# Kernel optimization log

Hardware: AMD Instinct MI355X
Metric: run time of the kernel (lower is better)

Reference implementation:

```python
import jax, jax.numpy as jnp
import numpy as np

B, N, M, C, H = 4, 8192, 8192, 512, 8
D = C // H  # head_dim = 64

def setup_inputs() -> dict:
    key = jax.random.key(0)
    ks = jax.random.split(key, 10)
    s = 1.0 / np.sqrt(C)
    return {
        "x": jax.random.normal(ks[0], (B, N, C), dtype=jnp.float32),
        "y": jax.random.normal(ks[1], (B, M, C), dtype=jnp.float32),
        "Wq": jax.random.normal(ks[2], (C, C), dtype=jnp.float32) * s,
        "bq": jax.random.normal(ks[3], (C,), dtype=jnp.float32) * s,
        "Wk": jax.random.normal(ks[4], (C, C), dtype=jnp.float32) * s,
        "bk": jax.random.normal(ks[5], (C,), dtype=jnp.float32) * s,
        "Wv": jax.random.normal(ks[6], (C, C), dtype=jnp.float32) * s,
        "bv": jax.random.normal(ks[7], (C,), dtype=jnp.float32) * s,
        "Wp": jax.random.normal(ks[8], (C, C), dtype=jnp.float32) * s,
        "bp": jax.random.normal(ks[9], (C,), dtype=jnp.float32) * s,
    }

def reference(x, y, Wq, bq, Wk, bk, Wv, bv, Wp, bp):
    # project and split heads: (B, S, C) -> (B, H, S, D)
    def heads(t, W, b, S):
        return (t @ W + b).reshape(B, S, H, D).transpose(0, 2, 1, 3)
    q = jax.nn.softmax(heads(x, Wq, bq, N), axis=-1)   # (B,H,N,D)
    k = jax.nn.softmax(heads(y, Wk, bk, M), axis=-1)   # (B,H,M,D)
    v = heads(y, Wv, bv, M)                             # (B,H,M,D)
    # denom: (q * sum_m k).sum_d, clamped
    ksum = jnp.sum(k, axis=2, keepdims=True)            # (B,H,1,D)
    denom = jnp.maximum(jnp.sum(q * ksum, axis=-1, keepdims=True), 1e-6)  # (B,H,N,1)
    # reassociated k^T @ v: (B,H,D,D), then q @ (k^T v)
    kv = jnp.einsum("bhmd,bhme->bhde", k, v)
    out = jnp.einsum("bhnd,bhde->bhne", q, kv) / denom + q  # (B,H,N,D)
    out = out.transpose(0, 2, 1, 3).reshape(B, N, C)
    return out @ Wp + bp  # dropout rate 0.0 -> identity
```

## Files before the change

### kernel.cpp

```cpp
#include <hip/hip_runtime.h>

typedef __bf16 bf16_t;
typedef __bf16 bf16x4 __attribute__((ext_vector_type(4)));
typedef __bf16 bf16x8 __attribute__((ext_vector_type(8)));
typedef float f32x4 __attribute__((ext_vector_type(4)));

#define AS1 __attribute__((address_space(1)))
#define AS3 __attribute__((address_space(3)))

__device__ __forceinline__ void gll16(const void* g, void* l) {
  __builtin_amdgcn_global_load_lds((AS1 void*)g, (AS3 void*)l, 16, 0, 0);
}

template <int ACT, bool TRANS>
__launch_bounds__(256, 2)
__global__ void gemm_k(const bf16_t* __restrict__ A, const bf16_t* __restrict__ BT,
                       const float* __restrict__ bias, void* __restrict__ Cout) {
  __shared__ __align__(16) bf16_t As[128 * 64];
  __shared__ __align__(16) bf16_t Bs[128 * 64];
  const int tid = threadIdx.x;
  const int lane = tid & 63, wid = tid >> 6;
  const int wr = wid >> 1, wc = wid & 1;
  const int rowbase = blockIdx.x * 128, colbase = blockIdx.y * 128;

  f32x4 zero = {0.f, 0.f, 0.f, 0.f};
  f32x4 acc[4][4];
#pragma unroll
  for (int i = 0; i < 4; ++i)
#pragma unroll
    for (int j = 0; j < 4; ++j) acc[i][j] = zero;

  const int srow = wid * 8 + (lane >> 3);
  const int scol = (lane & 7) * 8;
  const size_t abase = (size_t)(rowbase + srow) * 512 + scol;
  const size_t bbase = (size_t)(colbase + srow) * 512 + scol;
  bf16_t* lA = As + wid * 512;
  bf16_t* lB = Bs + wid * 512;

  for (int k0 = 0; k0 < 512; k0 += 64) {
#pragma unroll
    for (int i = 0; i < 4; ++i) {
      gll16(A + abase + (size_t)i * (32 * 512) + k0, lA + i * 2048);
      gll16(BT + bbase + (size_t)i * (32 * 512) + k0, lB + i * 2048);
    }
    __syncthreads();
#pragma unroll
    for (int kk = 0; kk < 64; kk += 32) {
      bf16x8 af[4], bfr[4];
#pragma unroll
      for (int ri = 0; ri < 4; ++ri)
        af[ri] = *(const bf16x8*)&As[(wr * 64 + ri * 16 + (lane & 15)) * 64 + kk + (lane >> 4) * 8];
#pragma unroll
      for (int ci = 0; ci < 4; ++ci)
        bfr[ci] = *(const bf16x8*)&Bs[(wc * 64 + ci * 16 + (lane & 15)) * 64 + kk + (lane >> 4) * 8];
#pragma unroll
      for (int ri = 0; ri < 4; ++ri)
#pragma unroll
        for (int ci = 0; ci < 4; ++ci)
          acc[ri][ci] = __builtin_amdgcn_mfma_f32_16x16x32_bf16(af[ri], bfr[ci], acc[ri][ci], 0, 0, 0);
    }
    __syncthreads();
  }

  float bb[4];
#pragma unroll
  for (int ci = 0; ci < 4; ++ci) bb[ci] = bias[colbase + wc * 64 + ci * 16 + (lane & 15)];
#pragma unroll
  for (int ri = 0; ri < 4; ++ri)
#pragma unroll
    for (int ci = 0; ci < 4; ++ci)
#pragma unroll
      for (int r = 0; r < 4; ++r) acc[ri][ci][r] += bb[ci];

  if (ACT == 1) {
#pragma unroll
    for (int ri = 0; ri < 4; ++ri) {
#pragma unroll
      for (int r = 0; r < 4; ++r) {
        float m = fmaxf(fmaxf(acc[ri][0][r], acc[ri][1][r]), fmaxf(acc[ri][2][r], acc[ri][3][r]));
        m = fmaxf(m, __shfl_xor(m, 1));
        m = fmaxf(m, __shfl_xor(m, 2));
        m = fmaxf(m, __shfl_xor(m, 4));
        m = fmaxf(m, __shfl_xor(m, 8));
        float s = 0.f;
#pragma unroll
        for (int ci = 0; ci < 4; ++ci) {
          float p = __expf(acc[ri][ci][r] - m);
          acc[ri][ci][r] = p;
          s += p;
        }
        s += __shfl_xor(s, 1);
        s += __shfl_xor(s, 2);
        s += __shfl_xor(s, 4);
        s += __shfl_xor(s, 8);
        float rcp = 1.0f / s;
#pragma unroll
        for (int ci = 0; ci < 4; ++ci) acc[ri][ci][r] *= rcp;
      }
    }
  }

  const int lr = (lane >> 4) * 4, lc = lane & 15;
#pragma unroll
  for (int ri = 0; ri < 4; ++ri)
#pragma unroll
    for (int ci = 0; ci < 4; ++ci)
#pragma unroll
      for (int r = 0; r < 4; ++r) {
        int gm = rowbase + wr * 64 + ri * 16 + lr + r;
        int c = colbase + wc * 64 + ci * 16 + lc;
        if (TRANS) {
          size_t idx = ((size_t)((gm >> 13) * 8 + (c >> 6)) * 64 + (c & 63)) * 8192 + (gm & 8191);
          ((bf16_t*)Cout)[idx] = (bf16_t)acc[ri][ci][r];
        } else {
          size_t idx = (size_t)gm * 512 + c;
          if (ACT == 2)
            ((float*)Cout)[idx] = acc[ri][ci][r];
          else
            ((bf16_t*)Cout)[idx] = (bf16_t)acc[ri][ci][r];
        }
      }
}

__launch_bounds__(256, 2)
__global__ void kv2_k(const bf16_t* __restrict__ Kt, const bf16_t* __restrict__ Vt,
                      float* __restrict__ kv, float* __restrict__ ksum) {
  __shared__ __align__(16) bf16_t Ks[64 * 64];
  __shared__ __align__(16) bf16_t Vs[64 * 64];
  const int bh = blockIdx.x >> 4, sp = blockIdx.x & 15;
  const int tid = threadIdx.x, lane = tid & 63, wid = tid >> 6;
  const size_t base = (size_t)bh * 64 * 8192;
  const int m0 = sp * 512;
  const int srow = wid * 8 + (lane >> 3);
  const int scol = (lane & 7) * 8;

  f32x4 zero = {0.f, 0.f, 0.f, 0.f};
  f32x4 acc[4], accs[4];
#pragma unroll
  for (int i = 0; i < 4; ++i) { acc[i] = zero; accs[i] = zero; }
  bf16x8 ones;
#pragma unroll
  for (int j = 0; j < 8; ++j) ones[j] = (bf16_t)1.0f;

  for (int c = 0; c < 8; ++c) {
    const int mc = m0 + c * 64;
#pragma unroll
    for (int i = 0; i < 2; ++i) {
      size_t g = base + (size_t)(srow + i * 32) * 8192 + mc + scol;
      gll16(Kt + g, Ks + wid * 512 + i * 2048);
      gll16(Vt + g, Vs + wid * 512 + i * 2048);
    }
    __syncthreads();
#pragma unroll
    for (int kk = 0; kk < 64; kk += 32) {
      bf16x8 af[4];
#pragma unroll
      for (int ri = 0; ri < 4; ++ri)
        af[ri] = *(const bf16x8*)&Ks[(ri * 16 + (lane & 15)) * 64 + kk + (lane >> 4) * 8];
      bf16x8 bfr = *(const bf16x8*)&Vs[(wid * 16 + (lane & 15)) * 64 + kk + (lane >> 4) * 8];
#pragma unroll
      for (int ri = 0; ri < 4; ++ri)
        acc[ri] = __builtin_amdgcn_mfma_f32_16x16x32_bf16(af[ri], bfr, acc[ri], 0, 0, 0);
      if (wid == 0) {
#pragma unroll
        for (int ri = 0; ri < 4; ++ri)
          accs[ri] = __builtin_amdgcn_mfma_f32_16x16x32_bf16(af[ri], ones, accs[ri], 0, 0, 0);
      }
    }
    __syncthreads();
  }

  const int lr = (lane >> 4) * 4, lc = lane & 15;
#pragma unroll
  for (int ri = 0; ri < 4; ++ri)
#pragma unroll
    for (int r = 0; r < 4; ++r)
      atomicAdd(&kv[((size_t)bh * 64 + ri * 16 + lr + r) * 64 + wid * 16 + lc], acc[ri][r]);
  if (wid == 0 && lc == 0) {
#pragma unroll
    for (int ri = 0; ri < 4; ++ri)
#pragma unroll
      for (int r = 0; r < 4; ++r)
        atomicAdd(&ksum[bh * 64 + ri * 16 + lr + r], accs[ri][r]);
  }
}

__global__ void build_kvB(const float* __restrict__ kv, const float* __restrict__ ksum,
                          bf16_t* __restrict__ kvB) {
  int i = blockIdx.x * 256 + threadIdx.x;
  if (i >= 32 * 80 * 64) return;
  int k = i & 63;
  int col = (i >> 6) % 80;
  int bh = i / (80 * 64);
  float v = 0.f;
  if (col < 64)
    v = kv[(size_t)(bh * 64 + k) * 64 + col];
  else if (col == 64)
    v = ksum[bh * 64 + k];
  kvB[i] = (bf16_t)v;
}

__launch_bounds__(256, 2)
__global__ void attn_k(const bf16_t* __restrict__ Q, const bf16_t* __restrict__ kvB,
                       bf16_t* __restrict__ attn) {
  __shared__ __align__(16) bf16_t As[128 * 64];
  const int rt = blockIdx.x;
  const int h = blockIdx.y;
  const int b = rt >> 6;
  const int bh = b * 8 + h;
  const int tid = threadIdx.x, lane = tid & 63, wid = tid >> 6;
  const int srow = wid * 8 + (lane >> 3);
  const int scol = (lane & 7) * 8;
#pragma unroll
  for (int i = 0; i < 4; ++i)
    gll16(Q + (size_t)(rt * 128 + srow + i * 32) * 512 + h * 64 + scol, As + wid * 512 + i * 2048);

  f32x4 zero = {0.f, 0.f, 0.f, 0.f};
  f32x4 acc[2][5];
#pragma unroll
  for (int i = 0; i < 2; ++i)
#pragma unroll
    for (int j = 0; j < 5; ++j) acc[i][j] = zero;
  __syncthreads();

  const bf16_t* Bb = kvB + (size_t)bh * (80 * 64);
#pragma unroll
  for (int kk = 0; kk < 64; kk += 32) {
    bf16x8 af[2];
#pragma unroll
    for (int ri = 0; ri < 2; ++ri)
      af[ri] = *(const bf16x8*)&As[(wid * 32 + ri * 16 + (lane & 15)) * 64 + kk + (lane >> 4) * 8];
#pragma unroll
    for (int ci = 0; ci < 5; ++ci) {
      bf16x8 bfr = *(const bf16x8*)&Bb[(ci * 16 + (lane & 15)) * 64 + kk + (lane >> 4) * 8];
#pragma unroll
      for (int ri = 0; ri < 2; ++ri)
        acc[ri][ci] = __builtin_amdgcn_mfma_f32_16x16x32_bf16(af[ri], bfr, acc[ri][ci], 0, 0, 0);
    }
  }

  const int lr = (lane >> 4) * 4, lc = lane & 15;
#pragma unroll
  for (int ri = 0; ri < 2; ++ri)
#pragma unroll
    for (int r = 0; r < 4; ++r) {
      float dn = __shfl(acc[ri][4][r], lane & 48);
      dn = fmaxf(dn, 1e-6f);
      float rinv = 1.0f / dn;
      int rl = wid * 32 + ri * 16 + lr + r;
#pragma unroll
      for (int ci = 0; ci < 4; ++ci) {
        int e = ci * 16 + lc;
        float qv = (float)As[rl * 64 + e];
        float o = acc[ri][ci][r] * rinv + qv;
        attn[(size_t)(rt * 128 + rl) * 512 + h * 64 + e] = (bf16_t)o;
      }
    }
}

__global__ void cvt_k(const float* __restrict__ in, bf16_t* __restrict__ out, int n4) {
  int i = blockIdx.x * blockDim.x + threadIdx.x;
  if (i < n4) {
    float4 v = ((const float4*)in)[i];
    bf16x4 o;
    o[0] = (bf16_t)v.x;
    o[1] = (bf16_t)v.y;
    o[2] = (bf16_t)v.z;
    o[3] = (bf16_t)v.w;
    ((bf16x4*)out)[i] = o;
  }
}

__global__ void wtrans_k(const float* __restrict__ W, bf16_t* __restrict__ WT) {
  int i = blockIdx.x * 256 + threadIdx.x;
  int n = i >> 9, k = i & 511;
  WT[i] = (bf16_t)W[k * 512 + n];
}

__global__ void zero_k(float* __restrict__ p, int n) {
  int i = blockIdx.x * 256 + threadIdx.x;
  if (i < n) p[i] = 0.f;
}

extern "C" void kernel_launch(void* const* d_in, const int* in_sizes, int n_in,
                              void* d_out, int out_size, void* d_ws, size_t ws_size,
                              hipStream_t stream) {
  (void)in_sizes; (void)n_in; (void)out_size; (void)ws_size;
  const float* x  = (const float*)d_in[0];
  const float* y  = (const float*)d_in[1];
  const float* Wq = (const float*)d_in[2];
  const float* bq = (const float*)d_in[3];
  const float* Wk = (const float*)d_in[4];
  const float* bk = (const float*)d_in[5];
  const float* Wv = (const float*)d_in[6];
  const float* bv = (const float*)d_in[7];
  const float* Wp = (const float*)d_in[8];
  const float* bp = (const float*)d_in[9];
  float* out = (float*)d_out;

  char* ws = (char*)d_ws;
  const size_t MB = 1024 * 1024;
  bf16_t* xbf = (bf16_t*)(ws + 0);
  bf16_t* ybf = (bf16_t*)(ws + 32 * MB);
  bf16_t* Qb  = (bf16_t*)(ws + 64 * MB);
  bf16_t* Kt  = (bf16_t*)(ws + 96 * MB);
  bf16_t* Vt  = (bf16_t*)(ws + 128 * MB);
  bf16_t* WqT = (bf16_t*)(ws + 160 * MB);
  bf16_t* WkT = WqT + 512 * 512;
  bf16_t* WvT = WkT + 512 * 512;
  bf16_t* WpT = WvT + 512 * 512;
  float* kv   = (float*)(ws + 163 * MB);
  float* ksum = kv + 32 * 64 * 64;
  bf16_t* kvB = (bf16_t*)(ws + 164 * MB);
  bf16_t* attn = xbf;

  cvt_k<<<16384, 256, 0, stream>>>(x, xbf, 4194304);
  cvt_k<<<16384, 256, 0, stream>>>(y, ybf, 4194304);
  wtrans_k<<<1024, 256, 0, stream>>>(Wq, WqT);
  wtrans_k<<<1024, 256, 0, stream>>>(Wk, WkT);
  wtrans_k<<<1024, 256, 0, stream>>>(Wv, WvT);
  wtrans_k<<<1024, 256, 0, stream>>>(Wp, WpT);

  dim3 gg(256, 4);
  gemm_k<1, false><<<gg, 256, 0, stream>>>(xbf, WqT, bq, Qb);
  gemm_k<1, true><<<gg, 256, 0, stream>>>(ybf, WkT, bk, Kt);
  gemm_k<0, true><<<gg, 256, 0, stream>>>(ybf, WvT, bv, Vt);

  zero_k<<<(133120 + 255) / 256, 256, 0, stream>>>(kv, 133120);
  kv2_k<<<512, 256, 0, stream>>>(Kt, Vt, kv, ksum);
  build_kvB<<<(32 * 80 * 64) / 256, 256, 0, stream>>>(kv, ksum, kvB);

  attn_k<<<dim3(256, 8), 256, 0, stream>>>(Qb, kvB, attn);

  gemm_k<2, false><<<gg, 256, 0, stream>>>(attn, WpT, bp, out);
}
```

Measured before the change: 357.3 us.

## Merge prep and QKV launches, replace kv atomics with split partials, vectorize K/V stores

The six conversion and transpose kernels become one prep kernel, and the three QKV projection GEMMs become one launch with a z-dimension selecting Q, K or V. The kv reduction now writes per-split partial buffers that build_kvB sums, which removes the atomics and the zero-init kernel. The transposed K/V epilogue now stores four consecutive bf16 values as one bf16x4 write instead of scalar scattered stores. This cuts launch overhead and store inefficiency, at the cost of a larger partial-sum workspace and a 16-way read in build_kvB.

```diff
diff --git a/kernel.cpp b/kernel.cpp
--- a/kernel.cpp
+++ b/kernel.cpp
@@ -13,15 +13,16 @@
 }
 
 template <int ACT, bool TRANS>
-__launch_bounds__(256, 2)
-__global__ void gemm_k(const bf16_t* __restrict__ A, const bf16_t* __restrict__ BT,
-                       const float* __restrict__ bias, void* __restrict__ Cout) {
+__device__ __forceinline__ void gemm_core(const bf16_t* __restrict__ A,
+                                          const bf16_t* __restrict__ BT,
+                                          const float* __restrict__ bias,
+                                          void* __restrict__ Cout,
+                                          int rowbase, int colbase) {
   __shared__ __align__(16) bf16_t As[128 * 64];
   __shared__ __align__(16) bf16_t Bs[128 * 64];
   const int tid = threadIdx.x;
   const int lane = tid & 63, wid = tid >> 6;
   const int wr = wid >> 1, wc = wid & 1;
-  const int rowbase = blockIdx.x * 128, colbase = blockIdx.y * 128;
 
   f32x4 zero = {0.f, 0.f, 0.f, 0.f};
   f32x4 acc[4][4];
@@ -101,30 +102,63 @@
   }
 
   const int lr = (lane >> 4) * 4, lc = lane & 15;
-#pragma unroll
-  for (int ri = 0; ri < 4; ++ri)
-#pragma unroll
-    for (int ci = 0; ci < 4; ++ci)
-#pragma unroll
-      for (int r = 0; r < 4; ++r) {
-        int gm = rowbase + wr * 64 + ri * 16 + lr + r;
+  if (TRANS) {
+#pragma unroll
+    for (int ri = 0; ri < 4; ++ri)
+#pragma unroll
+      for (int ci = 0; ci < 4; ++ci) {
+        bf16x4 pk;
+#pragma unroll
+        for (int r = 0; r < 4; ++r) pk[r] = (bf16_t)acc[ri][ci][r];
+        int gm0 = rowbase + wr * 64 + ri * 16 + lr;
         int c = colbase + wc * 64 + ci * 16 + lc;
-        if (TRANS) {
-          size_t idx = ((size_t)((gm >> 13) * 8 + (c >> 6)) * 64 + (c & 63)) * 8192 + (gm & 8191);
-          ((bf16_t*)Cout)[idx] = (bf16_t)acc[ri][ci][r];
-        } else {
+        size_t idx = ((size_t)((gm0 >> 13) * 8 + (c >> 6)) * 64 + (c & 63)) * 8192 + (gm0 & 8191);
+        *(bf16x4*)&((bf16_t*)Cout)[idx] = pk;
+      }
+  } else {
+#pragma unroll
+    for (int ri = 0; ri < 4; ++ri)
+#pragma unroll
+      for (int ci = 0; ci < 4; ++ci)
+#pragma unroll
+        for (int r = 0; r < 4; ++r) {
+          int gm = rowbase + wr * 64 + ri * 16 + lr + r;
+          int c = colbase + wc * 64 + ci * 16 + lc;
           size_t idx = (size_t)gm * 512 + c;
           if (ACT == 2)
             ((float*)Cout)[idx] = acc[ri][ci][r];
           else
             ((bf16_t*)Cout)[idx] = (bf16_t)acc[ri][ci][r];
         }
-      }
+  }
+}
+
+__launch_bounds__(256, 2)
+__global__ void qkv_k(const bf16_t* __restrict__ xbf, const bf16_t* __restrict__ ybf,
+                      const bf16_t* __restrict__ WqT, const bf16_t* __restrict__ WkT,
+                      const bf16_t* __restrict__ WvT,
+                      const float* __restrict__ bq, const float* __restrict__ bk,
+                      const float* __restrict__ bv,
+                      bf16_t* __restrict__ Qb, bf16_t* __restrict__ Kt,
+                      bf16_t* __restrict__ Vt) {
+  const int rowbase = blockIdx.x * 128, colbase = blockIdx.y * 128;
+  if (blockIdx.z == 0)
+    gemm_core<1, false>(xbf, WqT, bq, Qb, rowbase, colbase);
+  else if (blockIdx.z == 1)
+    gemm_core<1, true>(ybf, WkT, bk, Kt, rowbase, colbase);
+  else
+    gemm_core<0, true>(ybf, WvT, bv, Vt, rowbase, colbase);
+}
+
+__launch_bounds__(256, 2)
+__global__ void pgemm_k(const bf16_t* __restrict__ A, const bf16_t* __restrict__ BT,
+                        const float* __restrict__ bias, float* __restrict__ Cout) {
+  gemm_core<2, false>(A, BT, bias, Cout, blockIdx.x * 128, blockIdx.y * 128);
 }
 
 __launch_bounds__(256, 2)
 __global__ void kv2_k(const bf16_t* __restrict__ Kt, const bf16_t* __restrict__ Vt,
-                      float* __restrict__ kv, float* __restrict__ ksum) {
+                      float* __restrict__ kvp, float* __restrict__ ksp) {
   __shared__ __align__(16) bf16_t Ks[64 * 64];
   __shared__ __align__(16) bf16_t Vs[64 * 64];
   const int bh = blockIdx.x >> 4, sp = blockIdx.x & 15;
@@ -171,21 +205,22 @@
   }
 
   const int lr = (lane >> 4) * 4, lc = lane & 15;
+  float* o = kvp + ((size_t)sp * 32 + bh) * 4096;
 #pragma unroll
   for (int ri = 0; ri < 4; ++ri)
 #pragma unroll
     for (int r = 0; r < 4; ++r)
-      atomicAdd(&kv[((size_t)bh * 64 + ri * 16 + lr + r) * 64 + wid * 16 + lc], acc[ri][r]);
+      o[(ri * 16 + lr + r) * 64 + wid * 16 + lc] = acc[ri][r];
   if (wid == 0 && lc == 0) {
+    float* os = ksp + ((size_t)sp * 32 + bh) * 64;
 #pragma unroll
     for (int ri = 0; ri < 4; ++ri)
 #pragma unroll
-      for (int r = 0; r < 4; ++r)
-        atomicAdd(&ksum[bh * 64 + ri * 16 + lr + r], accs[ri][r]);
-  }
-}
-
-__global__ void build_kvB(const float* __restrict__ kv, const float* __restrict__ ksum,
+      for (int r = 0; r < 4; ++r) os[ri * 16 + lr + r] = accs[ri][r];
+  }
+}
+
+__global__ void build_kvB(const float* __restrict__ kvp, const float* __restrict__ ksp,
                           bf16_t* __restrict__ kvB) {
   int i = blockIdx.x * 256 + threadIdx.x;
   if (i >= 32 * 80 * 64) return;
@@ -193,10 +228,15 @@
   int col = (i >> 6) % 80;
   int bh = i / (80 * 64);
   float v = 0.f;
-  if (col < 64)
-    v = kv[(size_t)(bh * 64 + k) * 64 + col];
-  else if (col == 64)
-    v = ksum[bh * 64 + k];
+  if (col < 64) {
+#pragma unroll
+    for (int sp = 0; sp < 16; ++sp)
+      v += kvp[((size_t)sp * 32 + bh) * 4096 + k * 64 + col];
+  } else if (col == 64) {
+#pragma unroll
+    for (int sp = 0; sp < 16; ++sp)
+      v += ksp[((size_t)sp * 32 + bh) * 64 + k];
+  }
   kvB[i] = (bf16_t)v;
 }
 
@@ -258,28 +298,32 @@
     }
 }
 
-__global__ void cvt_k(const float* __restrict__ in, bf16_t* __restrict__ out, int n4) {
-  int i = blockIdx.x * blockDim.x + threadIdx.x;
-  if (i < n4) {
-    float4 v = ((const float4*)in)[i];
+__global__ void prep_k(const float* __restrict__ x, const float* __restrict__ y,
+                       const float* __restrict__ Wq, const float* __restrict__ Wk,
+                       const float* __restrict__ Wv, const float* __restrict__ Wp,
+                       bf16_t* __restrict__ xbf, bf16_t* __restrict__ ybf,
+                       bf16_t* __restrict__ WqT, bf16_t* __restrict__ WkT,
+                       bf16_t* __restrict__ WvT, bf16_t* __restrict__ WpT) {
+  int i = blockIdx.x * 256 + threadIdx.x;
+  if (i < 8388608) {
+    const float* src = (i < 4194304) ? x : y;
+    bf16_t* dst = (i < 4194304) ? xbf : ybf;
+    int j = (i < 4194304) ? i : i - 4194304;
+    float4 v = ((const float4*)src)[j];
     bf16x4 o;
     o[0] = (bf16_t)v.x;
     o[1] = (bf16_t)v.y;
     o[2] = (bf16_t)v.z;
     o[3] = (bf16_t)v.w;
-    ((bf16x4*)out)[i] = o;
-  }
-}
-
-__global__ void wtrans_k(const float* __restrict__ W, bf16_t* __restrict__ WT) {
-  int i = blockIdx.x * 256 + threadIdx.x;
-  int n = i >> 9, k = i & 511;
-  WT[i] = (bf16_t)W[k * 512 + n];
-}
-
-__global__ void zero_k(float* __restrict__ p, int n) {
-  int i = blockIdx.x * 256 + threadIdx.x;
-  if (i < n) p[i] = 0.f;
+    ((bf16x4*)dst)[j] = o;
+  } else {
+    int i2 = i - 8388608;
+    int w = i2 >> 18, j = i2 & 262143;
+    int n = j >> 9, k = j & 511;
+    const float* W = (w == 0) ? Wq : (w == 1) ? Wk : (w == 2) ? Wv : Wp;
+    bf16_t* WT = (w == 0) ? WqT : (w == 1) ? WkT : (w == 2) ? WvT : WpT;
+    WT[j] = (bf16_t)W[k * 512 + n];
+  }
 }
 
 extern "C" void kernel_launch(void* const* d_in, const int* in_sizes, int n_in,
@@ -309,28 +353,19 @@
   bf16_t* WkT = WqT + 512 * 512;
   bf16_t* WvT = WkT + 512 * 512;
   bf16_t* WpT = WvT + 512 * 512;
-  float* kv   = (float*)(ws + 163 * MB);
-  float* ksum = kv + 32 * 64 * 64;
-  bf16_t* kvB = (bf16_t*)(ws + 164 * MB);
+  float* kvp  = (float*)(ws + 163 * MB);
+  float* ksp  = (float*)(ws + 171 * MB);
+  bf16_t* kvB = (bf16_t*)(ws + 172 * MB);
   bf16_t* attn = xbf;
 
-  cvt_k<<<16384, 256, 0, stream>>>(x, xbf, 4194304);
-  cvt_k<<<16384, 256, 0, stream>>>(y, ybf, 4194304);
-  wtrans_k<<<1024, 256, 0, stream>>>(Wq, WqT);
-  wtrans_k<<<1024, 256, 0, stream>>>(Wk, WkT);
-  wtrans_k<<<1024, 256, 0, stream>>>(Wv, WvT);
-  wtrans_k<<<1024, 256, 0, stream>>>(Wp, WpT);
-
-  dim3 gg(256, 4);
-  gemm_k<1, false><<<gg, 256, 0, stream>>>(xbf, WqT, bq, Qb);
-  gemm_k<1, true><<<gg, 256, 0, stream>>>(ybf, WkT, bk, Kt);
-  gemm_k<0, true><<<gg, 256, 0, stream>>>(ybf, WvT, bv, Vt);
-
-  zero_k<<<(133120 + 255) / 256, 256, 0, stream>>>(kv, 133120);
-  kv2_k<<<512, 256, 0, stream>>>(Kt, Vt, kv, ksum);
-  build_kvB<<<(32 * 80 * 64) / 256, 256, 0, stream>>>(kv, ksum, kvB);
+  prep_k<<<36864, 256, 0, stream>>>(x, y, Wq, Wk, Wv, Wp, xbf, ybf, WqT, WkT, WvT, WpT);
+
+  qkv_k<<<dim3(256, 4, 3), 256, 0, stream>>>(xbf, ybf, WqT, WkT, WvT, bq, bk, bv, Qb, Kt, Vt);
+
+  kv2_k<<<512, 256, 0, stream>>>(Kt, Vt, kvp, ksp);
+  build_kvB<<<(32 * 80 * 64) / 256, 256, 0, stream>>>(kvp, ksp, kvB);
 
   attn_k<<<dim3(256, 8), 256, 0, stream>>>(Qb, kvB, attn);
 
-  gemm_k<2, false><<<gg, 256, 0, stream>>>(attn, WpT, bp, out);
-}
+  pgemm_k<<<dim3(256, 4), 256, 0, stream>>>(attn, WpT, bp, out);
+}
```

New measurement: 413.3 us. +15.7%, slower.
